# Optimization experiments

Measured on AMD Instinct MI355X. Metric: run time of the kernel, lower is better.

## Reference

```python
import jax, jax.numpy as jnp
import numpy as np

N_NODES = 100000
N_EDGES = 600000
IN_FEATS = 128
N_HIDDEN = 128
OUT_DIM = 64


def setup_inputs() -> dict:
    key = jax.random.key(0)
    ks = jax.random.split(key, 16)
    d = {
        "features": jax.random.normal(ks[0], (N_NODES, IN_FEATS), jnp.float32),
        "src": jax.random.randint(ks[1], (N_EDGES,), 0, N_NODES),
        "dst": jax.random.randint(ks[2], (N_EDGES,), 0, N_NODES),
    }
    def lin(k, fi, fo):
        return jax.random.normal(k, (fi, fo), jnp.float32) / np.sqrt(fi).astype(np.float32)
    dims = [(IN_FEATS, N_HIDDEN), (N_HIDDEN, N_HIDDEN), (N_HIDDEN, N_HIDDEN)]
    i = 3
    for l, (fi, fo) in enumerate(dims):
        d[f"W_self{l}"] = lin(ks[i], fi, fo); i += 1
        d[f"b_self{l}"] = jnp.zeros((fo,), jnp.float32)
        d[f"W_neigh{l}"] = lin(ks[i], fi, fo); i += 1
        d[f"b_neigh{l}"] = jnp.zeros((fo,), jnp.float32)
    d["W_out"] = lin(ks[i], N_HIDDEN, OUT_DIM)
    d["b_out"] = jnp.zeros((OUT_DIM,), jnp.float32)
    return d


def _sage_layer(h, src, dst, W_self, b_self, W_neigh, b_neigh, act):
    # DGL SAGEConv 'mean': aggregate neighbor feats (gather + segment mean),
    # then rst = fc_self(h) + fc_neigh(h_mean); activation afterwards.
    msg_sum = jax.ops.segment_sum(h[src], dst, num_segments=N_NODES)  # [N, F]
    deg = jax.ops.segment_sum(jnp.ones((src.shape[0], 1), h.dtype), dst,
                              num_segments=N_NODES)                   # [N, 1]
    h_neigh = msg_sum / jnp.maximum(deg, 1.0)  # nodes w/o in-edges -> 0
    out = (h @ W_self + b_self) + (h_neigh @ W_neigh + b_neigh)
    return jax.nn.relu(out) if act else out


def reference(features, src, dst,
              W_self0, b_self0, W_neigh0, b_neigh0,
              W_self1, b_self1, W_neigh1, b_neigh1,
              W_self2, b_self2, W_neigh2, b_neigh2,
              W_out, b_out):
    # feat_drop is identity in eval mode; direct=True path.
    h = _sage_layer(features, src, dst, W_self0, b_self0, W_neigh0, b_neigh0, True)
    h = _sage_layer(h, src, dst, W_self1, b_self1, W_neigh1, b_neigh1, True)
    h = _sage_layer(h, src, dst, W_self2, b_self2, W_neigh2, b_neigh2, False)
    return h @ W_out + b_out  # final_linear_single
```

## Files before the change

kernel.cpp:

```cpp
#include <hip/hip_runtime.h>

#define N_NODES 100000
#define N_EDGES 600000
#define F 128
#define OUTD 64
#define CAP 32

typedef short bf16x8 __attribute__((ext_vector_type(8)));
typedef float f32x4 __attribute__((ext_vector_type(4)));

__device__ __forceinline__ unsigned short f2bf(float f) {
    union { float f; unsigned u; } v; v.f = f;
    unsigned u = v.u;
    return (unsigned short)((u + 0x7FFFu + ((u >> 16) & 1u)) >> 16);
}
__device__ __forceinline__ float bf2f(unsigned short s) {
    union { unsigned u; float f; } v; v.u = ((unsigned)s) << 16;
    return v.f;
}

__device__ __forceinline__ void async_copy16(void* lds, const void* g) {
    __builtin_amdgcn_global_load_lds((const __attribute__((address_space(1))) void*)g,
                                     (__attribute__((address_space(3))) void*)lds, 16, 0, 0);
}

#define CVT_BLOCKS 12500
__global__ __launch_bounds__(256) void k_prep(const float4* __restrict__ feat4, ushort* __restrict__ h0,
                                              int* __restrict__ deg,
                                              const float* __restrict__ w0, const float* __restrict__ w1,
                                              const float* __restrict__ w2, const float* __restrict__ w3,
                                              const float* __restrict__ Ws2, const float* __restrict__ Wn2,
                                              const float* __restrict__ b2s, const float* __restrict__ b2n,
                                              const float* __restrict__ Wo, const float* __restrict__ bo,
                                              ushort* __restrict__ wt, ushort* __restrict__ wcs,
                                              ushort* __restrict__ wcn, float* __restrict__ bc) {
    int b = blockIdx.x, t = threadIdx.x;
    if (b < CVT_BLOCKS) {
        int i = b * 256 + t;
        float4 v = feat4[i];
        ushort4 o;
        o.x = f2bf(v.x); o.y = f2bf(v.y); o.z = f2bf(v.z); o.w = f2bf(v.w);
        *(ushort4*)&h0[i * 4] = o;
        if (i < N_NODES) deg[i] = 0;
    } else {
        int bb = b - CVT_BLOCKS;
        if (bb < 256) {
            int y = bb >> 6;
            int n = (bb & 63) * 2 + (t >> 7);
            int k = t & 127;
            const float* s = w0;
            if (y == 1) s = w1; else if (y == 2) s = w2; else if (y == 3) s = w3;
            wt[y * 16384 + n * 128 + k] = f2bf(s[k * 128 + n]);
        } else {
            int k = (bb - 256) * 2 + (t >> 7);
            int half = (t >> 6) & 1;
            int o = t & 63;
            const float* W2 = half ? Wn2 : Ws2;
            float s = 0.f;
#pragma unroll 4
            for (int j = 0; j < 128; ++j) s += W2[k * 128 + j] * Wo[j * 64 + o];
            (half ? wcn : wcs)[o * 128 + k] = f2bf(s);
            if (bb == 256 && t < 64) {
                float bsum = bo[o];
#pragma unroll 4
                for (int j = 0; j < 128; ++j) bsum += (b2s[j] + b2n[j]) * Wo[j * 64 + o];
                bc[o] = bsum;
            }
        }
    }
}

__global__ __launch_bounds__(256) void k_hist(const int* __restrict__ dst, int* __restrict__ deg,
                                              int* __restrict__ ord) {
    int e = blockIdx.x * blockDim.x + threadIdx.x;
    if (e < N_EDGES) ord[e] = atomicAdd(&deg[dst[e]], 1);
}

__global__ __launch_bounds__(256) void k_fill(const int* __restrict__ src, const int* __restrict__ dst,
                                              const int* __restrict__ ord, int* __restrict__ col) {
    int e = blockIdx.x * blockDim.x + threadIdx.x;
    if (e < N_EDGES) {
        col[dst[e] * CAP + ord[e]] = src[e];
    }
}

__device__ __forceinline__ void acc8(uint4 v, float* A) {
    A[0] += bf2f((unsigned short)(v.x & 0xFFFFu));
    A[1] += bf2f((unsigned short)(v.x >> 16));
    A[2] += bf2f((unsigned short)(v.y & 0xFFFFu));
    A[3] += bf2f((unsigned short)(v.y >> 16));
    A[4] += bf2f((unsigned short)(v.z & 0xFFFFu));
    A[5] += bf2f((unsigned short)(v.z >> 16));
    A[6] += bf2f((unsigned short)(v.w & 0xFFFFu));
    A[7] += bf2f((unsigned short)(v.w >> 16));
}

__global__ __launch_bounds__(256) void k_agg(const ushort* __restrict__ h, const int* __restrict__ deg,
                                             const int* __restrict__ col, ushort* __restrict__ out) {
    int gtid = blockIdx.x * blockDim.x + threadIdx.x;
    int node = gtid >> 4;
    int lane = threadIdx.x & 15;
    if (node >= N_NODES) return;
    int dg = deg[node];
    const int base = node * CAP;
    const uint4* hp = (const uint4*)h;
    float A[8] = {0.f, 0.f, 0.f, 0.f, 0.f, 0.f, 0.f, 0.f};
    float B[8] = {0.f, 0.f, 0.f, 0.f, 0.f, 0.f, 0.f, 0.f};
    int p = 0;
    for (; p + 4 <= dg; p += 4) {
        int c0 = col[base + p + 0], c1 = col[base + p + 1];
        int c2 = col[base + p + 2], c3 = col[base + p + 3];
        uint4 v0 = hp[(size_t)c0 * 16 + lane];
        uint4 v1 = hp[(size_t)c1 * 16 + lane];
        uint4 v2 = hp[(size_t)c2 * 16 + lane];
        uint4 v3 = hp[(size_t)c3 * 16 + lane];
        acc8(v0, A); acc8(v1, B); acc8(v2, A); acc8(v3, B);
    }
    for (; p < dg; ++p) {
        uint4 v = hp[(size_t)col[base + p] * 16 + lane];
        acc8(v, A);
    }
    float iv = 1.0f / (float)(dg > 0 ? dg : 1);
    uint4 o;
    o.x = (unsigned)f2bf((A[0] + B[0]) * iv) | ((unsigned)f2bf((A[1] + B[1]) * iv) << 16);
    o.y = (unsigned)f2bf((A[2] + B[2]) * iv) | ((unsigned)f2bf((A[3] + B[3]) * iv) << 16);
    o.z = (unsigned)f2bf((A[4] + B[4]) * iv) | ((unsigned)f2bf((A[5] + B[5]) * iv) << 16);
    o.w = (unsigned)f2bf((A[6] + B[6]) * iv) | ((unsigned)f2bf((A[7] + B[7]) * iv) << 16);
    ((uint4*)out)[(size_t)node * 16 + lane] = o;
}

template <int RELU>
__global__ __launch_bounds__(256) void k_gemm(const ushort* __restrict__ h, const ushort* __restrict__ hn,
                                              const ushort* __restrict__ Wts, const ushort* __restrict__ Wtn,
                                              const float* __restrict__ bs, const float* __restrict__ bn,
                                              ushort* __restrict__ out) {
    __shared__ ushort smem[16384];
    const int t = threadIdx.x;
    const int w = t >> 6, l = t & 63;
    const int wr = w >> 1, wc = w & 1;
    const int m0 = blockIdx.x * 128;

    f32x4 acc[4][4];
#pragma unroll
    for (int m = 0; m < 4; m++)
#pragma unroll
        for (int n = 0; n < 4; n++) acc[m][n] = (f32x4){0.f, 0.f, 0.f, 0.f};

    float bias[4];
#pragma unroll
    for (int n = 0; n < 4; n++) {
        int gc = wc * 64 + n * 16 + (l & 15);
        bias[n] = bs[gc] + bn[gc];
    }

    const int arow = t >> 2;
    const int acolsh = (t & 3) * 8;

#define STAGE(BUF, KT)                                                                            \
    do {                                                                                          \
        ushort* As_ = smem + (BUF) * 8192;                                                        \
        ushort* Bs_ = As_ + 4096;                                                                 \
        const ushort* Asrc = ((KT) < 4) ? h : hn;                                                 \
        const ushort* Bsrc = ((KT) < 4) ? Wts : Wtn;                                              \
        const int koff = ((KT) & 3) * 32;                                                         \
        _Pragma("unroll") for (int i = 0; i < 2; ++i) {                                           \
            int row = m0 + i * 64 + arow;                                                         \
            if (row > N_NODES - 1) row = N_NODES - 1;                                             \
            async_copy16(As_ + i * 2048 + w * 512, Asrc + (size_t)row * 128 + koff + acolsh);     \
            async_copy16(Bs_ + i * 2048 + w * 512,                                                \
                         Bsrc + (size_t)(i * 64 + arow) * 128 + koff + acolsh);                   \
        }                                                                                         \
    } while (0)

    STAGE(0, 0);
    for (int kt = 0; kt < 8; ++kt) {
        const int cur = kt & 1;
        if (kt < 7) {
            STAGE(cur ^ 1, kt + 1);
            asm volatile("s_waitcnt vmcnt(4)\n\ts_barrier" ::: "memory");
        } else {
            asm volatile("s_waitcnt vmcnt(0)\n\ts_barrier" ::: "memory");
        }
        const ushort* As = smem + cur * 8192;
        const ushort* Bs = As + 4096;
        const int kcol = (l >> 4) * 8;
        bf16x8 aF[4], bF[4];
#pragma unroll
        for (int m = 0; m < 4; m++) aF[m] = *(const bf16x8*)&As[(wr * 64 + m * 16 + (l & 15)) * 32 + kcol];
#pragma unroll
        for (int n = 0; n < 4; n++) bF[n] = *(const bf16x8*)&Bs[(wc * 64 + n * 16 + (l & 15)) * 32 + kcol];
#pragma unroll
        for (int m = 0; m < 4; m++)
#pragma unroll
            for (int n = 0; n < 4; n++)
                acc[m][n] = __builtin_amdgcn_mfma_f32_16x16x32_bf16(aF[m], bF[n], acc[m][n], 0, 0, 0);
        asm volatile("s_waitcnt lgkmcnt(0)\n\ts_barrier" ::: "memory");
    }
#undef STAGE
    __syncthreads();

    ushort* cw = smem + w * 4096;
#pragma unroll
    for (int m = 0; m < 4; m++)
#pragma unroll
        for (int n = 0; n < 4; n++) {
            int lr0 = m * 16 + (l >> 4) * 4;
            int lc = n * 16 + (l & 15);
#pragma unroll
            for (int j = 0; j < 4; j++) {
                float v = acc[m][n][j] + bias[n];
                if (RELU) v = fmaxf(v, 0.f);
                cw[(lr0 + j) * 64 + lc] = f2bf(v);
            }
        }
#pragma unroll
    for (int r = 0; r < 8; r++) {
        int row = r * 8 + (l >> 3);
        int cs = (l & 7) * 8;
        bf16x8 vv = *(const bf16x8*)&cw[row * 64 + cs];
        int grow = m0 + wr * 64 + row;
        if (grow < N_NODES) *(bf16x8*)&out[(size_t)grow * 128 + wc * 64 + cs] = vv;
    }
}

__global__ __launch_bounds__(256) void k_gemm_out(const ushort* __restrict__ h, const ushort* __restrict__ hn,
                                                  const ushort* __restrict__ Wcs, const ushort* __restrict__ Wcn,
                                                  const float* __restrict__ bc, float* __restrict__ out) {
    __shared__ ushort smem[16384];
    const int t = threadIdx.x;
    const int w = t >> 6, l = t & 63;
    const int wr = w >> 1, wc = w & 1;
    const int m0 = blockIdx.x * 128;

    f32x4 acc[4][2];
#pragma unroll
    for (int m = 0; m < 4; m++)
#pragma unroll
        for (int n = 0; n < 2; n++) acc[m][n] = (f32x4){0.f, 0.f, 0.f, 0.f};

    float bias[2];
#pragma unroll
    for (int n = 0; n < 2; n++) bias[n] = bc[wc * 32 + n * 16 + (l & 15)];

    const int arow = t >> 2;
    const int acolsh = (t & 3) * 8;

#define STAGEO(BUF, KT)                                                                          \
    do {                                                                                         \
        ushort* As_ = smem + (BUF) * 6144;                                                       \
        ushort* Bs_ = As_ + 4096;                                                                \
        const ushort* Asrc = ((KT) < 4) ? h : hn;                                                \
        const ushort* Bsrc = ((KT) < 4) ? Wcs : Wcn;                                             \
        const int koff = ((KT) & 3) * 32;                                                        \
        _Pragma("unroll") for (int i = 0; i < 2; ++i) {                                          \
            int row = m0 + i * 64 + arow;                                                        \
            if (row > N_NODES - 1) row = N_NODES - 1;                                            \
            async_copy16(As_ + i * 2048 + w * 512, Asrc + (size_t)row * 128 + koff + acolsh);    \
        }                                                                                        \
        async_copy16(Bs_ + w * 512, Bsrc + (size_t)arow * 128 + koff + acolsh);                  \
    } while (0)

    STAGEO(0, 0);
    for (int kt = 0; kt < 8; ++kt) {
        const int cur = kt & 1;
        if (kt < 7) {
            STAGEO(cur ^ 1, kt + 1);
            asm volatile("s_waitcnt vmcnt(3)\n\ts_barrier" ::: "memory");
        } else {
            asm volatile("s_waitcnt vmcnt(0)\n\ts_barrier" ::: "memory");
        }
        const ushort* As = smem + cur * 6144;
        const ushort* Bs = As + 4096;
        const int kcol = (l >> 4) * 8;
        bf16x8 aF[4], bF[2];
#pragma unroll
        for (int m = 0; m < 4; m++) aF[m] = *(const bf16x8*)&As[(wr * 64 + m * 16 + (l & 15)) * 32 + kcol];
#pragma unroll
        for (int n = 0; n < 2; n++) bF[n] = *(const bf16x8*)&Bs[(wc * 32 + n * 16 + (l & 15)) * 32 + kcol];
#pragma unroll
        for (int m = 0; m < 4; m++)
#pragma unroll
            for (int n = 0; n < 2; n++)
                acc[m][n] = __builtin_amdgcn_mfma_f32_16x16x32_bf16(aF[m], bF[n], acc[m][n], 0, 0, 0);
        asm volatile("s_waitcnt lgkmcnt(0)\n\ts_barrier" ::: "memory");
    }
#undef STAGEO
    __syncthreads();

    float* cw = (float*)smem + w * 2048;
#pragma unroll
    for (int m = 0; m < 4; m++)
#pragma unroll
        for (int n = 0; n < 2; n++) {
            int lr0 = m * 16 + (l >> 4) * 4;
            int lc = n * 16 + (l & 15);
#pragma unroll
            for (int j = 0; j < 4; j++) cw[(lr0 + j) * 32 + lc] = acc[m][n][j] + bias[n];
        }
#pragma unroll
    for (int r = 0; r < 8; r++) {
        int row = r * 8 + (l >> 3);
        int cf = (l & 7) * 4;
        float4 vv = *(const float4*)&cw[row * 32 + cf];
        int grow = m0 + wr * 64 + row;
        if (grow < N_NODES) *(float4*)&out[(size_t)grow * 64 + wc * 32 + cf] = vv;
    }
}

extern "C" void kernel_launch(void* const* d_in, const int* in_sizes, int n_in,
                              void* d_out, int out_size, void* d_ws, size_t ws_size,
                              hipStream_t stream) {
    const float* feat = (const float*)d_in[0];
    const int* src = (const int*)d_in[1];
    const int* dst = (const int*)d_in[2];
    const float* Wsf[3] = {(const float*)d_in[3], (const float*)d_in[7], (const float*)d_in[11]};
    const float* bsv[3] = {(const float*)d_in[4], (const float*)d_in[8], (const float*)d_in[12]};
    const float* Wnf[3] = {(const float*)d_in[5], (const float*)d_in[9], (const float*)d_in[13]};
    const float* bnv[3] = {(const float*)d_in[6], (const float*)d_in[10], (const float*)d_in[14]};
    const float* Wo = (const float*)d_in[15];
    const float* bo = (const float*)d_in[16];
    float* out = (float*)d_out;

    char* ws = (char*)d_ws;
    const size_t HB = (size_t)N_NODES * F * 2;
    ushort* h0 = (ushort*)ws;
    ushort* hA = (ushort*)(ws + HB);
    ushort* hB = (ushort*)(ws + 2 * HB);
    ushort* agg = (ushort*)(ws + 3 * HB);
    char* p = ws + 4 * HB;
    ushort* wt = (ushort*)p;       p += 4 * 16384 * 2;
    ushort* wcs = (ushort*)p;      p += 64 * 128 * 2;
    ushort* wcn = (ushort*)p;      p += 64 * 128 * 2;
    p = (char*)(((size_t)p + 255) & ~(size_t)255);
    float* bc = (float*)p;         p += 64 * 4 + 192;
    int* deg = (int*)p;            p += (size_t)N_NODES * 4;
    int* ord = (int*)p;            p += (size_t)N_EDGES * 4;
    int* col = (int*)p;

    const int edgeBlk = (N_EDGES + 255) / 256;

    k_prep<<<CVT_BLOCKS + 320, 256, 0, stream>>>((const float4*)feat, h0, deg,
                                                 Wsf[0], Wnf[0], Wsf[1], Wnf[1],
                                                 Wsf[2], Wnf[2], bsv[2], bnv[2], Wo, bo,
                                                 wt, wcs, wcn, bc);
    k_hist<<<edgeBlk, 256, 0, stream>>>(dst, deg, ord);
    k_fill<<<edgeBlk, 256, 0, stream>>>(src, dst, ord, col);

    const int aggBlk = (N_NODES * 16 + 255) / 256;
    const int gemmBlk = (N_NODES + 127) / 128;

    ushort* Wt0s = wt + 0 * 16384; ushort* Wt0n = wt + 1 * 16384;
    ushort* Wt1s = wt + 2 * 16384; ushort* Wt1n = wt + 3 * 16384;

    k_agg<<<aggBlk, 256, 0, stream>>>(h0, deg, col, agg);
    k_gemm<1><<<gemmBlk, 256, 0, stream>>>(h0, agg, Wt0s, Wt0n, bsv[0], bnv[0], hA);
    k_agg<<<aggBlk, 256, 0, stream>>>(hA, deg, col, agg);
    k_gemm<1><<<gemmBlk, 256, 0, stream>>>(hA, agg, Wt1s, Wt1n, bsv[1], bnv[1], hB);
    k_agg<<<aggBlk, 256, 0, stream>>>(hB, deg, col, agg);
    k_gemm_out<<<gemmBlk, 256, 0, stream>>>(hB, agg, wcs, wcn, bc, out);
}
```

Measured before the change: 200.0 us.

## Fuse neighbor aggregation into GEMM kernels via LDS-resident aggregated tile

```diff
diff --git a/kernel.cpp b/kernel.cpp
--- a/kernel.cpp
+++ b/kernel.cpp
@@ -95,51 +95,89 @@
     A[7] += bf2f((unsigned short)(v.w >> 16));
 }
 
-__global__ __launch_bounds__(256) void k_agg(const ushort* __restrict__ h, const int* __restrict__ deg,
-                                             const int* __restrict__ col, ushort* __restrict__ out) {
-    int gtid = blockIdx.x * blockDim.x + threadIdx.x;
-    int node = gtid >> 4;
-    int lane = threadIdx.x & 15;
-    if (node >= N_NODES) return;
-    int dg = deg[node];
-    const int base = node * CAP;
+__device__ __forceinline__ void agg_phase(const ushort* __restrict__ h, const int* __restrict__ deg,
+                                          const int* __restrict__ col, int m0, int t,
+                                          ushort* __restrict__ agg_lds) {
+    const int qw = t >> 4;
+    const int lane = t & 15;
     const uint4* hp = (const uint4*)h;
-    float A[8] = {0.f, 0.f, 0.f, 0.f, 0.f, 0.f, 0.f, 0.f};
-    float B[8] = {0.f, 0.f, 0.f, 0.f, 0.f, 0.f, 0.f, 0.f};
-    int p = 0;
-    for (; p + 4 <= dg; p += 4) {
-        int c0 = col[base + p + 0], c1 = col[base + p + 1];
-        int c2 = col[base + p + 2], c3 = col[base + p + 3];
-        uint4 v0 = hp[(size_t)c0 * 16 + lane];
-        uint4 v1 = hp[(size_t)c1 * 16 + lane];
-        uint4 v2 = hp[(size_t)c2 * 16 + lane];
-        uint4 v3 = hp[(size_t)c3 * 16 + lane];
-        acc8(v0, A); acc8(v1, B); acc8(v2, A); acc8(v3, B);
-    }
-    for (; p < dg; ++p) {
-        uint4 v = hp[(size_t)col[base + p] * 16 + lane];
-        acc8(v, A);
-    }
-    float iv = 1.0f / (float)(dg > 0 ? dg : 1);
-    uint4 o;
-    o.x = (unsigned)f2bf((A[0] + B[0]) * iv) | ((unsigned)f2bf((A[1] + B[1]) * iv) << 16);
-    o.y = (unsigned)f2bf((A[2] + B[2]) * iv) | ((unsigned)f2bf((A[3] + B[3]) * iv) << 16);
-    o.z = (unsigned)f2bf((A[4] + B[4]) * iv) | ((unsigned)f2bf((A[5] + B[5]) * iv) << 16);
-    o.w = (unsigned)f2bf((A[6] + B[6]) * iv) | ((unsigned)f2bf((A[7] + B[7]) * iv) << 16);
-    ((uint4*)out)[(size_t)node * 16 + lane] = o;
+#pragma unroll
+    for (int r8 = 0; r8 < 8; ++r8) {
+        int r = qw * 8 + r8;
+        int node = m0 + r;
+        if (node > N_NODES - 1) node = N_NODES - 1;
+        int dg = deg[node];
+        const int base = node * CAP;
+        float A[8] = {0.f, 0.f, 0.f, 0.f, 0.f, 0.f, 0.f, 0.f};
+        float B[8] = {0.f, 0.f, 0.f, 0.f, 0.f, 0.f, 0.f, 0.f};
+        int p = 0;
+        for (; p + 4 <= dg; p += 4) {
+            int c0 = col[base + p + 0], c1 = col[base + p + 1];
+            int c2 = col[base + p + 2], c3 = col[base + p + 3];
+            uint4 v0 = hp[(size_t)c0 * 16 + lane];
+            uint4 v1 = hp[(size_t)c1 * 16 + lane];
+            uint4 v2 = hp[(size_t)c2 * 16 + lane];
+            uint4 v3 = hp[(size_t)c3 * 16 + lane];
+            acc8(v0, A); acc8(v1, B); acc8(v2, A); acc8(v3, B);
+        }
+        for (; p < dg; ++p) {
+            uint4 v = hp[(size_t)col[base + p] * 16 + lane];
+            acc8(v, A);
+        }
+        float iv = 1.0f / (float)(dg > 0 ? dg : 1);
+        uint4 o;
+        o.x = (unsigned)f2bf((A[0] + B[0]) * iv) | ((unsigned)f2bf((A[1] + B[1]) * iv) << 16);
+        o.y = (unsigned)f2bf((A[2] + B[2]) * iv) | ((unsigned)f2bf((A[3] + B[3]) * iv) << 16);
+        o.z = (unsigned)f2bf((A[4] + B[4]) * iv) | ((unsigned)f2bf((A[5] + B[5]) * iv) << 16);
+        o.w = (unsigned)f2bf((A[6] + B[6]) * iv) | ((unsigned)f2bf((A[7] + B[7]) * iv) << 16);
+        *(uint4*)&agg_lds[lane * 1024 + r * 8] = o;
+    }
 }
 
 template <int RELU>
-__global__ __launch_bounds__(256) void k_gemm(const ushort* __restrict__ h, const ushort* __restrict__ hn,
-                                              const ushort* __restrict__ Wts, const ushort* __restrict__ Wtn,
-                                              const float* __restrict__ bs, const float* __restrict__ bn,
-                                              ushort* __restrict__ out) {
+__global__ __launch_bounds__(256) void k_agg_gemm(const ushort* __restrict__ h, const int* __restrict__ deg,
+                                                  const int* __restrict__ col,
+                                                  const ushort* __restrict__ Wts, const ushort* __restrict__ Wtn,
+                                                  const float* __restrict__ bs, const float* __restrict__ bn,
+                                                  ushort* __restrict__ out) {
+    __shared__ ushort agg_lds[16384];
     __shared__ ushort smem[16384];
     const int t = threadIdx.x;
     const int w = t >> 6, l = t & 63;
     const int wr = w >> 1, wc = w & 1;
     const int m0 = blockIdx.x * 128;
 
+    const int arow = t >> 2;
+    const int acolsh = (t & 3) * 8;
+
+#define STAGE_AB(BUF, KT)                                                                        \
+    do {                                                                                         \
+        ushort* As_ = smem + (BUF) * 8192;                                                       \
+        ushort* Bs_ = As_ + 4096;                                                                \
+        const int koff = (KT) * 32;                                                              \
+        _Pragma("unroll") for (int i = 0; i < 2; ++i) {                                          \
+            int row = m0 + i * 64 + arow;                                                        \
+            if (row > N_NODES - 1) row = N_NODES - 1;                                            \
+            async_copy16(As_ + i * 2048 + w * 512, h + (size_t)row * 128 + koff + acolsh);       \
+            async_copy16(Bs_ + i * 2048 + w * 512,                                               \
+                         Wts + (size_t)(i * 64 + arow) * 128 + koff + acolsh);                   \
+        }                                                                                        \
+    } while (0)
+
+#define STAGE_B(BUF, KT)                                                                         \
+    do {                                                                                         \
+        ushort* Bs_ = smem + (BUF) * 8192 + 4096;                                                \
+        const int koff = ((KT) & 3) * 32;                                                        \
+        _Pragma("unroll") for (int i = 0; i < 2; ++i) {                                          \
+            async_copy16(Bs_ + i * 2048 + w * 512,                                               \
+                         Wtn + (size_t)(i * 64 + arow) * 128 + koff + acolsh);                   \
+        }                                                                                        \
+    } while (0)
+
+    STAGE_AB(0, 0);
+    agg_phase(h, deg, col, m0, t, agg_lds);
+    __syncthreads();
+
     f32x4 acc[4][4];
 #pragma unroll
     for (int m = 0; m < 4; m++)
@@ -153,40 +191,33 @@
         bias[n] = bs[gc] + bn[gc];
     }
 
-    const int arow = t >> 2;
-    const int acolsh = (t & 3) * 8;
-
-#define STAGE(BUF, KT)                                                                            \
-    do {                                                                                          \
-        ushort* As_ = smem + (BUF) * 8192;                                                        \
-        ushort* Bs_ = As_ + 4096;                                                                 \
-        const ushort* Asrc = ((KT) < 4) ? h : hn;                                                 \
-        const ushort* Bsrc = ((KT) < 4) ? Wts : Wtn;                                              \
-        const int koff = ((KT) & 3) * 32;                                                         \
-        _Pragma("unroll") for (int i = 0; i < 2; ++i) {                                           \
-            int row = m0 + i * 64 + arow;                                                         \
-            if (row > N_NODES - 1) row = N_NODES - 1;                                             \
-            async_copy16(As_ + i * 2048 + w * 512, Asrc + (size_t)row * 128 + koff + acolsh);     \
-            async_copy16(Bs_ + i * 2048 + w * 512,                                                \
-                         Bsrc + (size_t)(i * 64 + arow) * 128 + koff + acolsh);                   \
-        }                                                                                         \
-    } while (0)
-
-    STAGE(0, 0);
     for (int kt = 0; kt < 8; ++kt) {
         const int cur = kt & 1;
-        if (kt < 7) {
-            STAGE(cur ^ 1, kt + 1);
+        if (kt < 3) {
+            STAGE_AB(cur ^ 1, kt + 1);
             asm volatile("s_waitcnt vmcnt(4)\n\ts_barrier" ::: "memory");
+        } else if (kt < 7) {
+            STAGE_B(cur ^ 1, kt + 1);
+            asm volatile("s_waitcnt vmcnt(2)\n\ts_barrier" ::: "memory");
         } else {
             asm volatile("s_waitcnt vmcnt(0)\n\ts_barrier" ::: "memory");
         }
-        const ushort* As = smem + cur * 8192;
-        const ushort* Bs = As + 4096;
         const int kcol = (l >> 4) * 8;
         bf16x8 aF[4], bF[4];
-#pragma unroll
-        for (int m = 0; m < 4; m++) aF[m] = *(const bf16x8*)&As[(wr * 64 + m * 16 + (l & 15)) * 32 + kcol];
+        if (kt < 4) {
+            const ushort* As = smem + cur * 8192;
+#pragma unroll
+            for (int m = 0; m < 4; m++)
+                aF[m] = *(const bf16x8*)&As[(wr * 64 + m * 16 + (l & 15)) * 32 + kcol];
+        } else {
+            const int slot = (kt & 3) * 4 + (l >> 4);
+#pragma unroll
+            for (int m = 0; m < 4; m++) {
+                int r = wr * 64 + m * 16 + (l & 15);
+                aF[m] = *(const bf16x8*)&agg_lds[slot * 1024 + r * 8];
+            }
+        }
+        const ushort* Bs = smem + cur * 8192 + 4096;
 #pragma unroll
         for (int n = 0; n < 4; n++) bF[n] = *(const bf16x8*)&Bs[(wc * 64 + n * 16 + (l & 15)) * 32 + kcol];
 #pragma unroll
@@ -196,7 +227,8 @@
                 acc[m][n] = __builtin_amdgcn_mfma_f32_16x16x32_bf16(aF[m], bF[n], acc[m][n], 0, 0, 0);
         asm volatile("s_waitcnt lgkmcnt(0)\n\ts_barrier" ::: "memory");
     }
-#undef STAGE
+#undef STAGE_AB
+#undef STAGE_B
     __syncthreads();
 
     ushort* cw = smem + w * 4096;
@@ -223,58 +255,81 @@
     }
 }
 
-__global__ __launch_bounds__(256) void k_gemm_out(const ushort* __restrict__ h, const ushort* __restrict__ hn,
-                                                  const ushort* __restrict__ Wcs, const ushort* __restrict__ Wcn,
-                                                  const float* __restrict__ bc, float* __restrict__ out) {
+__global__ __launch_bounds__(256) void k_agg_gemm_out(const ushort* __restrict__ h, const int* __restrict__ deg,
+                                                       const int* __restrict__ col,
+                                                       const ushort* __restrict__ Wcs, const ushort* __restrict__ Wcn,
+                                                       const float* __restrict__ bc, float* __restrict__ out) {
+    __shared__ ushort agg_lds[16384];
     __shared__ ushort smem[16384];
     const int t = threadIdx.x;
     const int w = t >> 6, l = t & 63;
     const int wr = w >> 1, wc = w & 1;
     const int m0 = blockIdx.x * 128;
 
-    f32x4 acc[4][2];
-#pragma unroll
-    for (int m = 0; m < 4; m++)
-#pragma unroll
-        for (int n = 0; n < 2; n++) acc[m][n] = (f32x4){0.f, 0.f, 0.f, 0.f};
-
-    float bias[2];
-#pragma unroll
-    for (int n = 0; n < 2; n++) bias[n] = bc[wc * 32 + n * 16 + (l & 15)];
-
     const int arow = t >> 2;
     const int acolsh = (t & 3) * 8;
 
-#define STAGEO(BUF, KT)                                                                          \
+#define STAGEO_AB(BUF, KT)                                                                       \
     do {                                                                                         \
         ushort* As_ = smem + (BUF) * 6144;                                                       \
         ushort* Bs_ = As_ + 4096;                                                                \
-        const ushort* Asrc = ((KT) < 4) ? h : hn;                                                \
-        const ushort* Bsrc = ((KT) < 4) ? Wcs : Wcn;                                             \
-        const int koff = ((KT) & 3) * 32;                                                        \
+        const int koff = (KT) * 32;                                                              \
         _Pragma("unroll") for (int i = 0; i < 2; ++i) {                                          \
             int row = m0 + i * 64 + arow;                                                        \
             if (row > N_NODES - 1) row = N_NODES - 1;                                            \
-            async_copy16(As_ + i * 2048 + w * 512, Asrc + (size_t)row * 128 + koff + acolsh);    \
+            async_copy16(As_ + i * 2048 + w * 512, h + (size_t)row * 128 + koff + acolsh);       \
         }                                                                                        \
-        async_copy16(Bs_ + w * 512, Bsrc + (size_t)arow * 128 + koff + acolsh);                  \
+        async_copy16(Bs_ + w * 512, Wcs + (size_t)arow * 128 + koff + acolsh);                   \
     } while (0)
 
-    STAGEO(0, 0);
+#define STAGEO_B(BUF, KT)                                                                        \
+    do {                                                                                         \
+        ushort* Bs_ = smem + (BUF) * 6144 + 4096;                                                \
+        const int koff = ((KT) & 3) * 32;                                                        \
+        async_copy16(Bs_ + w * 512, Wcn + (size_t)arow * 128 + koff + acolsh);                   \
+    } while (0)
+
+    STAGEO_AB(0, 0);
+    agg_phase(h, deg, col, m0, t, agg_lds);
+    __syncthreads();
+
+    f32x4 acc[4][2];
+#pragma unroll
+    for (int m = 0; m < 4; m++)
+#pragma unroll
+        for (int n = 0; n < 2; n++) acc[m][n] = (f32x4){0.f, 0.f, 0.f, 0.f};
+
+    float bias[2];
+#pragma unroll
+    for (int n = 0; n < 2; n++) bias[n] = bc[wc * 32 + n * 16 + (l & 15)];
+
     for (int kt = 0; kt < 8; ++kt) {
         const int cur = kt & 1;
-        if (kt < 7) {
-            STAGEO(cur ^ 1, kt + 1);
+        if (kt < 3) {
+            STAGEO_AB(cur ^ 1, kt + 1);
             asm volatile("s_waitcnt vmcnt(3)\n\ts_barrier" ::: "memory");
+        } else if (kt < 7) {
+            STAGEO_B(cur ^ 1, kt + 1);
+            asm volatile("s_waitcnt vmcnt(1)\n\ts_barrier" ::: "memory");
         } else {
             asm volatile("s_waitcnt vmcnt(0)\n\ts_barrier" ::: "memory");
         }
-        const ushort* As = smem + cur * 6144;
-        const ushort* Bs = As + 4096;
         const int kcol = (l >> 4) * 8;
         bf16x8 aF[4], bF[2];
-#pragma unroll
-        for (int m = 0; m < 4; m++) aF[m] = *(const bf16x8*)&As[(wr * 64 + m * 16 + (l & 15)) * 32 + kcol];
+        if (kt < 4) {
+            const ushort* As = smem + cur * 6144;
+#pragma unroll
+            for (int m = 0; m < 4; m++)
+                aF[m] = *(const bf16x8*)&As[(wr * 64 + m * 16 + (l & 15)) * 32 + kcol];
+        } else {
+            const int slot = (kt & 3) * 4 + (l >> 4);
+#pragma unroll
+            for (int m = 0; m < 4; m++) {
+                int r = wr * 64 + m * 16 + (l & 15);
+                aF[m] = *(const bf16x8*)&agg_lds[slot * 1024 + r * 8];
+            }
+        }
+        const ushort* Bs = smem + cur * 6144 + 4096;
 #pragma unroll
         for (int n = 0; n < 2; n++) bF[n] = *(const bf16x8*)&Bs[(wc * 32 + n * 16 + (l & 15)) * 32 + kcol];
 #pragma unroll
@@ -284,7 +339,8 @@
                 acc[m][n] = __builtin_amdgcn_mfma_f32_16x16x32_bf16(aF[m], bF[n], acc[m][n], 0, 0, 0);
         asm volatile("s_waitcnt lgkmcnt(0)\n\ts_barrier" ::: "memory");
     }
-#undef STAGEO
+#undef STAGEO_AB
+#undef STAGEO_B
     __syncthreads();
 
     float* cw = (float*)smem + w * 2048;
@@ -326,8 +382,7 @@
     ushort* h0 = (ushort*)ws;
     ushort* hA = (ushort*)(ws + HB);
     ushort* hB = (ushort*)(ws + 2 * HB);
-    ushort* agg = (ushort*)(ws + 3 * HB);
-    char* p = ws + 4 * HB;
+    char* p = ws + 3 * HB;
     ushort* wt = (ushort*)p;       p += 4 * 16384 * 2;
     ushort* wcs = (ushort*)p;      p += 64 * 128 * 2;
     ushort* wcn = (ushort*)p;      p += 64 * 128 * 2;
@@ -346,16 +401,12 @@
     k_hist<<<edgeBlk, 256, 0, stream>>>(dst, deg, ord);
     k_fill<<<edgeBlk, 256, 0, stream>>>(src, dst, ord, col);
 
-    const int aggBlk = (N_NODES * 16 + 255) / 256;
     const int gemmBlk = (N_NODES + 127) / 128;
 
     ushort* Wt0s = wt + 0 * 16384; ushort* Wt0n = wt + 1 * 16384;
     ushort* Wt1s = wt + 2 * 16384; ushort* Wt1n = wt + 3 * 16384;
 
-    k_agg<<<aggBlk, 256, 0, stream>>>(h0, deg, col, agg);
-    k_gemm<1><<<gemmBlk, 256, 0, stream>>>(h0, agg, Wt0s, Wt0n, bsv[0], bnv[0], hA);
-    k_agg<<<aggBlk, 256, 0, stream>>>(hA, deg, col, agg);
-    k_gemm<1><<<gemmBlk, 256, 0, stream>>>(hA, agg, Wt1s, Wt1n, bsv[1], bnv[1], hB);
-    k_agg<<<aggBlk, 256, 0, stream>>>(hB, deg, col, agg);
-    k_gemm_out<<<gemmBlk, 256, 0, stream>>>(hB, agg, wcs, wcn, bc, out);
-}
+    k_agg_gemm<1><<<gemmBlk, 256, 0, stream>>>(h0, deg, col, Wt0s, Wt0n, bsv[0], bnv[0], hA);
+    k_agg_gemm<1><<<gemmBlk, 256, 0, stream>>>(hA, deg, col, Wt1s, Wt1n, bsv[1], bnv[1], hB);
+    k_agg_gemm_out<<<gemmBlk, 256, 0, stream>>>(hB, deg, col, wcs, wcn, bc, out);
+}
```

Measured after the change: 272.3 us. +36.1%, slower.
